# Optimization experiments

Measured on AMD Instinct MI355X. Metric: run time of the kernel, lower is better.

Reference implementation:

```python
import jax, jax.numpy as jnp
import numpy as np

N = 100000   # total nodes (batched graphs)
E = 800000   # random edges (self-loops appended -> E+N total)
G = 2000     # number of graphs in batch
H = 4        # heads per GAT layer
D = 64       # hidden_size (per-head out dim)
IN = 64      # in_feats
EXTRA = 8    # extra graph-level feats
HID = H * D  # 256


def setup_inputs() -> dict:
    key = jax.random.key(0)
    ks = jax.random.split(key, 24)
    s = 0.5  # init std used in the torch module
    feats_node = jax.random.normal(ks[0], (N, IN), jnp.float32)
    feats_graph = jax.random.normal(ks[1], (G, EXTRA), jnp.float32)
    # edges + self loops (DGL GATConv requires no zero-in-degree nodes)
    src = jnp.concatenate([jax.random.randint(ks[2], (E,), 0, N), jnp.arange(N)])
    dst = jnp.concatenate([jax.random.randint(ks[3], (E,), 0, N), jnp.arange(N)])
    node_gid = jnp.sort(jax.random.randint(ks[4], (N,), 0, G))
    # GAT layer 1
    W1 = jax.random.normal(ks[5], (IN, HID), jnp.float32) * s
    al1 = jax.random.normal(ks[6], (H, D), jnp.float32) * s
    ar1 = jax.random.normal(ks[7], (H, D), jnp.float32) * s
    b1 = jnp.zeros((HID,), jnp.float32)
    # GAT layer 2
    W2 = jax.random.normal(ks[8], (HID, HID), jnp.float32) * s
    al2 = jax.random.normal(ks[9], (H, D), jnp.float32) * s
    ar2 = jax.random.normal(ks[10], (H, D), jnp.float32) * s
    b2 = jnp.zeros((HID,), jnp.float32)
    # WeightedAverage readout score
    Ws = jax.random.normal(ks[11], (HID, 1), jnp.float32) * s
    bs = jnp.zeros((1,), jnp.float32)
    # MLP: 264 -> 128 -> 64 -> 1 with SELU
    Wm1 = jax.random.normal(ks[12], (HID + EXTRA, 2 * D), jnp.float32) * s
    bm1 = jnp.zeros((2 * D,), jnp.float32)
    Wm2 = jax.random.normal(ks[13], (2 * D, D), jnp.float32) * s
    bm2 = jnp.zeros((D,), jnp.float32)
    Wm3 = jax.random.normal(ks[14], (D, 1), jnp.float32) * s
    bm3 = jnp.zeros((1,), jnp.float32)
    return dict(feats_node=feats_node, feats_graph=feats_graph,
                W1=W1, al1=al1, ar1=ar1, b1=b1,
                W2=W2, al2=al2, ar2=ar2, b2=b2,
                Ws=Ws, bs=bs, Wm1=Wm1, bm1=bm1, Wm2=Wm2, bm2=bm2,
                Wm3=Wm3, bm3=bm3,
                src=src, dst=dst, node_gid=node_gid)


def gat_layer(x, W, al, ar, b, src, dst):
    # DGL GATConv: fc -> per-node attn projections -> edge leaky_relu ->
    # edge softmax over incoming edges -> weighted scatter-sum -> +bias
    f = (x @ W).reshape(N, H, D)                       # [N,H,D]
    el = jnp.einsum('nhd,hd->nh', f, al)               # [N,H]
    er = jnp.einsum('nhd,hd->nh', f, ar)               # [N,H]
    e = jax.nn.leaky_relu(el[src] + er[dst], 0.2)      # [E',H]
    m = jax.ops.segment_max(e, dst, num_segments=N)    # per-dst max
    e = jnp.exp(e - m[dst])
    denom = jax.ops.segment_sum(e, dst, num_segments=N)
    alpha = e / denom[dst]                             # edge softmax [E',H]
    out = jax.ops.segment_sum(alpha[:, :, None] * f[src], dst, num_segments=N)
    return out.reshape(N, HID) + b


def reference(feats_node, feats_graph, W1, al1, ar1, b1, W2, al2, ar2, b2,
              Ws, bs, Wm1, bm1, Wm2, bm2, Wm3, bm3, src, dst, node_gid):
    x = jax.nn.relu(gat_layer(feats_node, W1, al1, ar1, b1, src, dst))
    x = jax.nn.relu(gat_layer(x, W2, al2, ar2, b2, src, dst))
    # weighted-average readout per graph: sum(w*x)/sum(w)
    w = jax.nn.sigmoid(x @ Ws + bs)                    # [N,1]
    num = jax.ops.segment_sum(w * x, node_gid, num_segments=G)
    den = jax.ops.segment_sum(w, node_gid, num_segments=G)
    emb = num / jnp.where(den == 0, 1.0, den)          # [G,HID]
    h = jnp.concatenate([emb, feats_graph], axis=1)    # [G,HID+EXTRA]
    h = jax.nn.selu(h @ Wm1 + bm1)
    h = jax.nn.selu(h @ Wm2 + bm2)
    return h @ Wm3 + bm3                               # [G,1]
```

## Files before the change

kernel.cpp:

```cpp
#include <hip/hip_runtime.h>
#include <hip/hip_bf16.h>
#include <math.h>

#define NN     100000
#define GG     2000
#define HH     4
#define DD     64
#define HID    256
#define INF_   64
#define EXTRA  8

typedef unsigned short u16;
typedef __attribute__((ext_vector_type(8))) short bf16x8;
typedef __attribute__((ext_vector_type(4))) float f32x4;

__device__ __forceinline__ u16 f2bf(float f) {
    unsigned u = __float_as_uint(f);
    return (u16)((u + 0x7fffu + ((u >> 16) & 1u)) >> 16);
}
__device__ __forceinline__ float bf2f(u16 v) {
    return __uint_as_float(((unsigned)v) << 16);
}

__global__ __launch_bounds__(256) void wsplit_kernel(
    const float* __restrict__ W, u16* __restrict__ hi, u16* __restrict__ lo,
    int K, int lgK)
{
    int idx = blockIdx.x * 256 + threadIdx.x;
    if (idx >= 256 * K) return;
    int n = idx >> lgK, k = idx & (K - 1);
    float w = W[k * HID + n];
    u16 h = f2bf(w);
    hi[idx] = h;
    lo[idx] = f2bf(w - bf2f(h));
}

template<bool BF16_OUT>
__global__ __launch_bounds__(256) void mfma_gemm_kernel(
    const float* __restrict__ A, const u16* __restrict__ BThi,
    const u16* __restrict__ BTlo, float* __restrict__ Cf, u16* __restrict__ Cb,
    const float* __restrict__ al, const float* __restrict__ ar,
    float* __restrict__ el, float* __restrict__ er, int M, int K)
{
    __shared__ __align__(16) u16 Ah[128 * 40];
    __shared__ __align__(16) u16 Al[128 * 40];
    __shared__ __align__(16) u16 Bh[128 * 40];
    __shared__ __align__(16) u16 Bl[128 * 40];
    const int tid  = threadIdx.x;
    const int wave = tid >> 6, lane = tid & 63;
    const int quad = lane >> 4, l15 = lane & 15;
    const int wy = wave >> 1, wx = wave & 1;
    const int r0 = blockIdx.x * 128, c0 = blockIdx.y * 128;
    const int sr = tid >> 2, sseg = tid & 3;

    f32x4 acc[4][4];
    #pragma unroll
    for (int i = 0; i < 4; ++i)
        #pragma unroll
        for (int j = 0; j < 4; ++j)
            acc[i][j] = (f32x4){0.f, 0.f, 0.f, 0.f};

    for (int k0 = 0; k0 < K; k0 += 32) {
        #pragma unroll
        for (int half = 0; half < 2; ++half) {
            int r = sr + half * 64;
            int gr = min(r0 + r, M - 1);
            const float* ap = A + (size_t)gr * K + k0 + sseg * 8;
            float4 va0 = *reinterpret_cast<const float4*>(ap);
            float4 va1 = *reinterpret_cast<const float4*>(ap + 4);
            float av[8] = {va0.x, va0.y, va0.z, va0.w, va1.x, va1.y, va1.z, va1.w};
            bf16x8 vh, vl;
            #pragma unroll
            for (int m = 0; m < 8; ++m) {
                u16 h = f2bf(av[m]);
                vh[m] = (short)h;
                vl[m] = (short)f2bf(av[m] - bf2f(h));
            }
            *reinterpret_cast<bf16x8*>(&Ah[r * 40 + sseg * 8]) = vh;
            *reinterpret_cast<bf16x8*>(&Al[r * 40 + sseg * 8]) = vl;
            int gc = c0 + r;
            *reinterpret_cast<bf16x8*>(&Bh[r * 40 + sseg * 8]) =
                *reinterpret_cast<const bf16x8*>(BThi + (size_t)gc * K + k0 + sseg * 8);
            *reinterpret_cast<bf16x8*>(&Bl[r * 40 + sseg * 8]) =
                *reinterpret_cast<const bf16x8*>(BTlo + (size_t)gc * K + k0 + sseg * 8);
        }
        __syncthreads();
        bf16x8 afh[4], afl[4], bfh[4], bfl[4];
        #pragma unroll
        for (int i = 0; i < 4; ++i) {
            int row = (wy * 64 + i * 16 + l15) * 40 + quad * 8;
            afh[i] = *reinterpret_cast<const bf16x8*>(&Ah[row]);
            afl[i] = *reinterpret_cast<const bf16x8*>(&Al[row]);
        }
        #pragma unroll
        for (int j = 0; j < 4; ++j) {
            int row = (wx * 64 + j * 16 + l15) * 40 + quad * 8;
            bfh[j] = *reinterpret_cast<const bf16x8*>(&Bh[row]);
            bfl[j] = *reinterpret_cast<const bf16x8*>(&Bl[row]);
        }
        #pragma unroll
        for (int i = 0; i < 4; ++i)
            #pragma unroll
            for (int j = 0; j < 4; ++j) {
                acc[i][j] = __builtin_amdgcn_mfma_f32_16x16x32_bf16(afh[i], bfh[j], acc[i][j], 0, 0, 0);
                acc[i][j] = __builtin_amdgcn_mfma_f32_16x16x32_bf16(afl[i], bfh[j], acc[i][j], 0, 0, 0);
                acc[i][j] = __builtin_amdgcn_mfma_f32_16x16x32_bf16(afh[i], bfl[j], acc[i][j], 0, 0, 0);
            }
        __syncthreads();
    }

    #pragma unroll
    for (int i = 0; i < 4; ++i)
        #pragma unroll
        for (int rr = 0; rr < 4; ++rr) {
            int grow = r0 + wy * 64 + i * 16 + quad * 4 + rr;
            if (grow < M) {
                if (BF16_OUT) {
                    u16* crow = Cb + (size_t)grow * HID + c0 + wx * 64 + l15;
                    #pragma unroll
                    for (int j = 0; j < 4; ++j) crow[j * 16] = f2bf(acc[i][j][rr]);
                } else {
                    float* crow = Cf + (size_t)grow * HID + c0 + wx * 64 + l15;
                    #pragma unroll
                    for (int j = 0; j < 4; ++j) crow[j * 16] = acc[i][j][rr];
                }
            }
        }

    const int h = blockIdx.y * 2 + wx;
    float alf[4], arf[4];
    #pragma unroll
    for (int j = 0; j < 4; ++j) {
        alf[j] = al[h * DD + j * 16 + l15];
        arf[j] = ar[h * DD + j * 16 + l15];
    }
    #pragma unroll
    for (int i = 0; i < 4; ++i)
        #pragma unroll
        for (int rr = 0; rr < 4; ++rr) {
            float sl = acc[i][0][rr] * alf[0] + acc[i][1][rr] * alf[1]
                     + acc[i][2][rr] * alf[2] + acc[i][3][rr] * alf[3];
            float sr_ = acc[i][0][rr] * arf[0] + acc[i][1][rr] * arf[1]
                      + acc[i][2][rr] * arf[2] + acc[i][3][rr] * arf[3];
            #pragma unroll
            for (int off = 1; off < 16; off <<= 1) {
                sl  += __shfl_xor(sl, off, 64);
                sr_ += __shfl_xor(sr_, off, 64);
            }
            if (l15 == 0) {
                int grow = r0 + wy * 64 + i * 16 + quad * 4 + rr;
                if (grow < M) {
                    el[grow * 4 + h] = sl;
                    er[grow * 4 + h] = sr_;
                }
            }
        }
}

__device__ __forceinline__ float leaky02(float x) { return x > 0.f ? x : 0.2f * x; }

__global__ __launch_bounds__(256) void edge_softmax_kernel(
    const float* __restrict__ el, const float* __restrict__ er,
    const int* __restrict__ rowptr, const int* __restrict__ colsrc,
    float* __restrict__ w, float* __restrict__ invden)
{
    int idx = blockIdx.x * 256 + threadIdx.x;
    if (idx >= NN * HH) return;
    int t = idx >> 2, h = idx & 3;
    int beg = rowptr[t], end = rowptr[t + 1];
    float ert = er[idx];
    float m = -1e30f;
    for (int i = beg; i < end; ++i) {
        int s = colsrc[i];
        m = fmaxf(m, leaky02(el[s * 4 + h] + ert));
    }
    float den = 0.f;
    for (int i = beg; i < end; ++i) {
        int s = colsrc[i];
        float v = expf(leaky02(el[s * 4 + h] + ert) - m);
        w[(size_t)i * 4 + h] = v;
        den += v;
    }
    invden[idx] = 1.f / den;
}

__global__ __launch_bounds__(256) void aggregate_f32_kernel(
    const float* __restrict__ F, const float* __restrict__ w,
    const float* __restrict__ invden, const int* __restrict__ rowptr,
    const int* __restrict__ colsrc, const float* __restrict__ bias,
    float* __restrict__ out)
{
    int t = blockIdx.x * 4 + (threadIdx.x >> 6);
    int lane = threadIdx.x & 63;
    if (t >= NN) return;
    int beg = rowptr[t], end = rowptr[t + 1];
    const int h = lane >> 4;
    float4 acc0 = make_float4(0.f, 0.f, 0.f, 0.f);
    float4 acc1 = make_float4(0.f, 0.f, 0.f, 0.f);
    int i = beg;
    for (; i + 1 < end; i += 2) {
        int s0 = colsrc[i], s1 = colsrc[i + 1];
        float w0 = w[(size_t)i * 4 + h];
        float w1 = w[(size_t)(i + 1) * 4 + h];
        float4 f0 = *reinterpret_cast<const float4*>(F + (size_t)s0 * HID + 4 * lane);
        float4 f1 = *reinterpret_cast<const float4*>(F + (size_t)s1 * HID + 4 * lane);
        acc0.x += w0 * f0.x; acc0.y += w0 * f0.y; acc0.z += w0 * f0.z; acc0.w += w0 * f0.w;
        acc1.x += w1 * f1.x; acc1.y += w1 * f1.y; acc1.z += w1 * f1.z; acc1.w += w1 * f1.w;
    }
    if (i < end) {
        int s0 = colsrc[i];
        float w0 = w[(size_t)i * 4 + h];
        float4 f0 = *reinterpret_cast<const float4*>(F + (size_t)s0 * HID + 4 * lane);
        acc0.x += w0 * f0.x; acc0.y += w0 * f0.y; acc0.z += w0 * f0.z; acc0.w += w0 * f0.w;
    }
    float inv = invden[t * 4 + h];
    float4 bv = *reinterpret_cast<const float4*>(bias + 4 * lane);
    float4 r;
    r.x = fmaxf((acc0.x + acc1.x) * inv + bv.x, 0.f);
    r.y = fmaxf((acc0.y + acc1.y) * inv + bv.y, 0.f);
    r.z = fmaxf((acc0.z + acc1.z) * inv + bv.z, 0.f);
    r.w = fmaxf((acc0.w + acc1.w) * inv + bv.w, 0.f);
    *reinterpret_cast<float4*>(out + (size_t)t * HID + 4 * lane) = r;
}

__global__ __launch_bounds__(256) void aggregate_bf16_kernel(
    const u16* __restrict__ F, const float* __restrict__ w,
    const float* __restrict__ invden, const int* __restrict__ rowptr,
    const int* __restrict__ colsrc, const float* __restrict__ bias,
    u16* __restrict__ out)
{
    int t = blockIdx.x * 4 + (threadIdx.x >> 6);
    int lane = threadIdx.x & 63;
    if (t >= NN) return;
    int beg = rowptr[t], end = rowptr[t + 1];
    const int h = lane >> 4;
    float4 acc0 = make_float4(0.f, 0.f, 0.f, 0.f);
    float4 acc1 = make_float4(0.f, 0.f, 0.f, 0.f);
    int i = beg;
    for (; i + 1 < end; i += 2) {
        int s0 = colsrc[i], s1 = colsrc[i + 1];
        float w0 = w[(size_t)i * 4 + h];
        float w1 = w[(size_t)(i + 1) * 4 + h];
        ushort4 f0 = *reinterpret_cast<const ushort4*>(F + (size_t)s0 * HID + 4 * lane);
        ushort4 f1 = *reinterpret_cast<const ushort4*>(F + (size_t)s1 * HID + 4 * lane);
        acc0.x += w0 * bf2f(f0.x); acc0.y += w0 * bf2f(f0.y);
        acc0.z += w0 * bf2f(f0.z); acc0.w += w0 * bf2f(f0.w);
        acc1.x += w1 * bf2f(f1.x); acc1.y += w1 * bf2f(f1.y);
        acc1.z += w1 * bf2f(f1.z); acc1.w += w1 * bf2f(f1.w);
    }
    if (i < end) {
        int s0 = colsrc[i];
        float w0 = w[(size_t)i * 4 + h];
        ushort4 f0 = *reinterpret_cast<const ushort4*>(F + (size_t)s0 * HID + 4 * lane);
        acc0.x += w0 * bf2f(f0.x); acc0.y += w0 * bf2f(f0.y);
        acc0.z += w0 * bf2f(f0.z); acc0.w += w0 * bf2f(f0.w);
    }
    float inv = invden[t * 4 + h];
    float4 bv = *reinterpret_cast<const float4*>(bias + 4 * lane);
    ushort4 r;
    r.x = f2bf(fmaxf((acc0.x + acc1.x) * inv + bv.x, 0.f));
    r.y = f2bf(fmaxf((acc0.y + acc1.y) * inv + bv.y, 0.f));
    r.z = f2bf(fmaxf((acc0.z + acc1.z) * inv + bv.z, 0.f));
    r.w = f2bf(fmaxf((acc0.w + acc1.w) * inv + bv.w, 0.f));
    *reinterpret_cast<ushort4*>(out + (size_t)t * HID + 4 * lane) = r;
}

__global__ __launch_bounds__(256) void readout_kernel(
    const u16* __restrict__ X, const float* __restrict__ Ws,
    const float* __restrict__ bs, const int* __restrict__ gptr,
    float* __restrict__ emb)
{
    int g = blockIdx.x * 4 + (threadIdx.x >> 6);
    int lane = threadIdx.x & 63;
    if (g >= GG) return;
    int beg = gptr[g], end = gptr[g + 1];
    float4 wv = *reinterpret_cast<const float4*>(Ws + 4 * lane);
    float b = bs[0];
    float4 acc = make_float4(0.f, 0.f, 0.f, 0.f);
    float wsum = 0.f;
    for (int n = beg; n < end; ++n) {
        ushort4 xv = *reinterpret_cast<const ushort4*>(X + (size_t)n * HID + 4 * lane);
        float x0 = bf2f(xv.x), x1 = bf2f(xv.y), x2 = bf2f(xv.z), x3 = bf2f(xv.w);
        float p = x0 * wv.x + x1 * wv.y + x2 * wv.z + x3 * wv.w;
        #pragma unroll
        for (int off = 32; off; off >>= 1) p += __shfl_xor(p, off, 64);
        float w = 1.f / (1.f + expf(-(p + b)));
        wsum += w;
        acc.x += w * x0; acc.y += w * x1; acc.z += w * x2; acc.w += w * x3;
    }
    float inv = (wsum == 0.f) ? 1.f : wsum;
    float4 e;
    e.x = acc.x / inv; e.y = acc.y / inv; e.z = acc.z / inv; e.w = acc.w / inv;
    *reinterpret_cast<float4*>(emb + (size_t)g * HID + 4 * lane) = e;
}

__device__ __forceinline__ float selu_f(float x)
{
    const float scale = 1.0507009873554805f, alpha = 1.6732632423543772f;
    return scale * (x > 0.f ? x : alpha * expm1f(x));
}

__global__ __launch_bounds__(128) void mlp_kernel(
    const float* __restrict__ emb, const float* __restrict__ fg,
    const float* __restrict__ Wm1, const float* __restrict__ bm1,
    const float* __restrict__ Wm2, const float* __restrict__ bm2,
    const float* __restrict__ Wm3, const float* __restrict__ bm3,
    float* __restrict__ out)
{
    int g = blockIdx.x;
    __shared__ float h[HID + EXTRA];
    __shared__ float h1[128];
    __shared__ float h2[64];
    int tid = threadIdx.x;
    h[tid] = emb[(size_t)g * HID + tid];
    h[128 + tid] = emb[(size_t)g * HID + 128 + tid];
    if (tid < EXTRA) h[HID + tid] = fg[(size_t)g * EXTRA + tid];
    __syncthreads();
    float acc = bm1[tid];
    for (int i = 0; i < HID + EXTRA; ++i) acc += h[i] * Wm1[i * 128 + tid];
    h1[tid] = selu_f(acc);
    __syncthreads();
    if (tid < 64) {
        float acc2 = bm2[tid];
        for (int i = 0; i < 128; ++i) acc2 += h1[i] * Wm2[i * 64 + tid];
        h2[tid] = selu_f(acc2);
    }
    __syncthreads();
    if (tid < 64) {
        float p = h2[tid] * Wm3[tid];
        #pragma unroll
        for (int off = 32; off; off >>= 1) p += __shfl_xor(p, off, 64);
        if (tid == 0) out[g] = p + bm3[0];
    }
}

__global__ void count_dst_kernel(const int* __restrict__ dst, int* __restrict__ cnt, int E)
{
    int e = blockIdx.x * 256 + threadIdx.x;
    if (e < E) atomicAdd(&cnt[dst[e]], 1);
}
__global__ void count_gid_kernel(const int* __restrict__ gid, int* __restrict__ cnt, int n)
{
    int i = blockIdx.x * 256 + threadIdx.x;
    if (i < n) atomicAdd(&cnt[gid[i]], 1);
}
__global__ void fill_csr_kernel(const int* __restrict__ src, const int* __restrict__ dst,
                                int* __restrict__ cursor, int* __restrict__ colsrc, int E)
{
    int e = blockIdx.x * 256 + threadIdx.x;
    if (e < E) {
        int p = atomicAdd(&cursor[dst[e]], 1);
        colsrc[p] = src[e];
    }
}

__global__ __launch_bounds__(256) void scan_blocks_kernel(
    const int* __restrict__ in, int n, int* __restrict__ out, int* __restrict__ partials)
{
    __shared__ int lds[256];
    int tid = threadIdx.x;
    int base = blockIdx.x * 1024 + tid * 4;
    int v0 = (base + 0 < n) ? in[base + 0] : 0;
    int v1 = (base + 1 < n) ? in[base + 1] : 0;
    int v2 = (base + 2 < n) ? in[base + 2] : 0;
    int v3 = (base + 3 < n) ? in[base + 3] : 0;
    int s = v0 + v1 + v2 + v3;
    lds[tid] = s;
    __syncthreads();
    for (int off = 1; off < 256; off <<= 1) {
        int t = (tid >= off) ? lds[tid - off] : 0;
        __syncthreads();
        lds[tid] += t;
        __syncthreads();
    }
    int excl = lds[tid] - s;
    if (base + 0 < n) out[base + 0] = excl;
    if (base + 1 < n) out[base + 1] = excl + v0;
    if (base + 2 < n) out[base + 2] = excl + v0 + v1;
    if (base + 3 < n) out[base + 3] = excl + v0 + v1 + v2;
    if (tid == 255) partials[blockIdx.x] = lds[255];
}

__global__ __launch_bounds__(256) void scan_partials_kernel(int* partials, int nb)
{
    __shared__ int lds[256];
    int tid = threadIdx.x;
    int v = (tid < nb) ? partials[tid] : 0;
    lds[tid] = v;
    __syncthreads();
    for (int off = 1; off < 256; off <<= 1) {
        int t = (tid >= off) ? lds[tid - off] : 0;
        __syncthreads();
        lds[tid] += t;
        __syncthreads();
    }
    int excl = lds[tid] - v;
    if (tid < nb) partials[tid] = excl;
}

__global__ void add_offsets_kernel(int* __restrict__ out, const int* __restrict__ partials, int n)
{
    int i = blockIdx.x * 256 + threadIdx.x;
    if (i < n) out[i] += partials[i >> 10];
}

extern "C" void kernel_launch(void* const* d_in, const int* in_sizes, int n_in,
                              void* d_out, int out_size, void* d_ws, size_t ws_size,
                              hipStream_t stream)
{
    const float* feats_node  = (const float*)d_in[0];
    const float* feats_graph = (const float*)d_in[1];
    const float* W1  = (const float*)d_in[2];
    const float* al1 = (const float*)d_in[3];
    const float* ar1 = (const float*)d_in[4];
    const float* b1  = (const float*)d_in[5];
    const float* W2  = (const float*)d_in[6];
    const float* al2 = (const float*)d_in[7];
    const float* ar2 = (const float*)d_in[8];
    const float* b2  = (const float*)d_in[9];
    const float* Ws  = (const float*)d_in[10];
    const float* bs  = (const float*)d_in[11];
    const float* Wm1 = (const float*)d_in[12];
    const float* bm1 = (const float*)d_in[13];
    const float* Wm2 = (const float*)d_in[14];
    const float* bm2 = (const float*)d_in[15];
    const float* Wm3 = (const float*)d_in[16];
    const float* bm3 = (const float*)d_in[17];
    const int* src = (const int*)d_in[18];
    const int* dst = (const int*)d_in[19];
    const int* gid = (const int*)d_in[20];
    float* out = (float*)d_out;
    const int E = in_sizes[18];

    char* p = (char*)d_ws;
    auto alloc = [&](size_t bytes) {
        char* r = p;
        p += (bytes + 255) & ~(size_t)255;
        return r;
    };
    float* F      = (float*)alloc((size_t)NN * HID * 4);
    float* X      = (float*)alloc((size_t)NN * HID * 4);
    float* el     = (float*)alloc((size_t)NN * HH * 4);
    float* er     = (float*)alloc((size_t)NN * HH * 4);
    float* wbuf   = (float*)alloc((size_t)E * HH * 4);
    float* invden = (float*)alloc((size_t)NN * HH * 4);
    int*   cnt    = (int*)alloc((size_t)(NN + 1) * 4);
    int*   rowptr = (int*)alloc((size_t)(NN + 1) * 4);
    int*   colsrc = (int*)alloc((size_t)E * 4);
    int*   gcnt   = (int*)alloc((size_t)(GG + 1) * 4);
    int*   gptr   = (int*)alloc((size_t)(GG + 1) * 4);
    int*   parts  = (int*)alloc(1024 * 4);
    float* emb    = (float*)alloc((size_t)GG * HID * 4);
    u16*   BT1h   = (u16*)alloc((size_t)HID * INF_ * 2);
    u16*   BT1l   = (u16*)alloc((size_t)HID * INF_ * 2);
    u16*   BT2h   = (u16*)alloc((size_t)HID * HID * 2);
    u16*   BT2l   = (u16*)alloc((size_t)HID * HID * 2);
    u16*   Fbf2   = (u16*)F;
    u16*   Xbf2   = (u16*)X;

    hipMemsetAsync(cnt, 0, (size_t)(NN + 1) * 4, stream);
    count_dst_kernel<<<(E + 255) / 256, 256, 0, stream>>>(dst, cnt, E);
    {
        int n = NN + 1, nb = (n + 1023) / 1024;
        scan_blocks_kernel<<<nb, 256, 0, stream>>>(cnt, n, rowptr, parts);
        scan_partials_kernel<<<1, 256, 0, stream>>>(parts, nb);
        add_offsets_kernel<<<(n + 255) / 256, 256, 0, stream>>>(rowptr, parts, n);
    }
    hipMemcpyAsync(cnt, rowptr, (size_t)(NN + 1) * 4, hipMemcpyDeviceToDevice, stream);
    fill_csr_kernel<<<(E + 255) / 256, 256, 0, stream>>>(src, dst, cnt, colsrc, E);

    hipMemsetAsync(gcnt, 0, (size_t)(GG + 1) * 4, stream);
    count_gid_kernel<<<(NN + 255) / 256, 256, 0, stream>>>(gid, gcnt, NN);
    {
        int n = GG + 1, nb = (n + 1023) / 1024;
        scan_blocks_kernel<<<nb, 256, 0, stream>>>(gcnt, n, gptr, parts);
        scan_partials_kernel<<<1, 256, 0, stream>>>(parts, nb);
        add_offsets_kernel<<<(n + 255) / 256, 256, 0, stream>>>(gptr, parts, n);
    }

    wsplit_kernel<<<(HID * INF_ + 255) / 256, 256, 0, stream>>>(W1, BT1h, BT1l, INF_, 6);
    wsplit_kernel<<<(HID * HID + 255) / 256, 256, 0, stream>>>(W2, BT2h, BT2l, HID, 8);

    dim3 ggrid((NN + 127) / 128, HID / 128);
    const int nh_blocks = (NN * HH + 255) / 256;

    mfma_gemm_kernel<false><<<ggrid, 256, 0, stream>>>(
        feats_node, BT1h, BT1l, F, nullptr, al1, ar1, el, er, NN, INF_);
    edge_softmax_kernel<<<nh_blocks, 256, 0, stream>>>(el, er, rowptr, colsrc, wbuf, invden);
    aggregate_f32_kernel<<<(NN + 3) / 4, 256, 0, stream>>>(F, wbuf, invden, rowptr, colsrc, b1, X);

    mfma_gemm_kernel<true><<<ggrid, 256, 0, stream>>>(
        X, BT2h, BT2l, nullptr, Fbf2, al2, ar2, el, er, NN, HID);
    edge_softmax_kernel<<<nh_blocks, 256, 0, stream>>>(el, er, rowptr, colsrc, wbuf, invden);
    aggregate_bf16_kernel<<<(NN + 3) / 4, 256, 0, stream>>>(Fbf2, wbuf, invden, rowptr, colsrc,
                                                            b2, Xbf2);

    readout_kernel<<<(GG + 3) / 4, 256, 0, stream>>>(Xbf2, Ws, bs, gptr, emb);
    mlp_kernel<<<GG, 128, 0, stream>>>(emb, feats_graph, Wm1, bm1, Wm2, bm2, Wm3, bm3, out);
}
```

Baseline: 671.6 us.

## Aggregate raw 64-wide features before layer-1 projection and fold attention into weights

Layer 1 is reordered so attention logits are computed directly from input features using W1·al and W1·ar precomputed vectors. Neighbor aggregation then gathers 64-float input rows instead of 256-float projected rows, producing per-head aggregated inputs. A new per-head MFMA GEMM applies W1 with bias and ReLU afterwards. This cuts gather traffic in the first aggregation about fourfold, at the cost of writing and re-reading a full 256-wide intermediate and adding a few kernels.

```diff
diff --git a/kernel.cpp b/kernel.cpp
--- a/kernel.cpp
+++ b/kernel.cpp
@@ -33,6 +33,143 @@
     u16 h = f2bf(w);
     hi[idx] = h;
     lo[idx] = f2bf(w - bf2f(h));
+}
+
+__global__ __launch_bounds__(256) void walprep_kernel(
+    const float* __restrict__ W1, const float* __restrict__ al,
+    const float* __restrict__ ar, float* __restrict__ wal, float* __restrict__ war)
+{
+    int tid = threadIdx.x;
+    int d = tid >> 2, h = tid & 3;
+    const float* wrow = W1 + d * HID + h * DD;
+    const float* av = al + h * DD;
+    const float* bv = ar + h * DD;
+    float s1 = 0.f, s2 = 0.f;
+    for (int c = 0; c < DD; ++c) { s1 += wrow[c] * av[c]; s2 += wrow[c] * bv[c]; }
+    wal[d * 4 + h] = s1;
+    war[d * 4 + h] = s2;
+}
+
+__global__ __launch_bounds__(256) void elr1_kernel(
+    const float* __restrict__ feats, const float* __restrict__ wal,
+    const float* __restrict__ war, float* __restrict__ el, float* __restrict__ er)
+{
+    int idx = blockIdx.x * 256 + threadIdx.x;
+    if (idx >= NN * HH) return;
+    int n = idx >> 2, h = idx & 3;
+    const float* f = feats + (size_t)n * INF_;
+    float s1 = 0.f, s2 = 0.f;
+    #pragma unroll 4
+    for (int d = 0; d < INF_; d += 4) {
+        float4 fv = *reinterpret_cast<const float4*>(f + d);
+        s1 += fv.x * wal[(d + 0) * 4 + h] + fv.y * wal[(d + 1) * 4 + h]
+            + fv.z * wal[(d + 2) * 4 + h] + fv.w * wal[(d + 3) * 4 + h];
+        s2 += fv.x * war[(d + 0) * 4 + h] + fv.y * war[(d + 1) * 4 + h]
+            + fv.z * war[(d + 2) * 4 + h] + fv.w * war[(d + 3) * 4 + h];
+    }
+    el[idx] = s1;
+    er[idx] = s2;
+}
+
+__global__ __launch_bounds__(256) void aggregate_feats_kernel(
+    const float* __restrict__ feats, const float* __restrict__ w,
+    const float* __restrict__ invden, const int* __restrict__ rowptr,
+    const int* __restrict__ colsrc, float* __restrict__ Y1)
+{
+    int t = blockIdx.x * 4 + (threadIdx.x >> 6);
+    int lane = threadIdx.x & 63;
+    if (t >= NN) return;
+    int beg = rowptr[t], end = rowptr[t + 1];
+    float a0 = 0.f, a1 = 0.f, a2 = 0.f, a3 = 0.f;
+    float b0 = 0.f, b1 = 0.f, b2 = 0.f, b3 = 0.f;
+    int i = beg;
+    for (; i + 1 < end; i += 2) {
+        int s0 = colsrc[i], s1 = colsrc[i + 1];
+        float4 w0 = *reinterpret_cast<const float4*>(w + (size_t)i * 4);
+        float4 w1 = *reinterpret_cast<const float4*>(w + (size_t)(i + 1) * 4);
+        float f0 = feats[(size_t)s0 * INF_ + lane];
+        float f1 = feats[(size_t)s1 * INF_ + lane];
+        a0 += w0.x * f0; a1 += w0.y * f0; a2 += w0.z * f0; a3 += w0.w * f0;
+        b0 += w1.x * f1; b1 += w1.y * f1; b2 += w1.z * f1; b3 += w1.w * f1;
+    }
+    if (i < end) {
+        int s0 = colsrc[i];
+        float4 w0 = *reinterpret_cast<const float4*>(w + (size_t)i * 4);
+        float f0 = feats[(size_t)s0 * INF_ + lane];
+        a0 += w0.x * f0; a1 += w0.y * f0; a2 += w0.z * f0; a3 += w0.w * f0;
+    }
+    float4 inv = *reinterpret_cast<const float4*>(invden + (size_t)t * 4);
+    float* y = Y1 + (size_t)t * HID;
+    y[lane]       = (a0 + b0) * inv.x;
+    y[64 + lane]  = (a1 + b1) * inv.y;
+    y[128 + lane] = (a2 + b2) * inv.z;
+    y[192 + lane] = (a3 + b3) * inv.w;
+}
+
+__global__ __launch_bounds__(256) void gemm_head_kernel(
+    const float* __restrict__ Y1, const u16* __restrict__ BThi,
+    const u16* __restrict__ BTlo, const float* __restrict__ bias,
+    float* __restrict__ X1, int M)
+{
+    const int tid  = threadIdx.x;
+    const int wv   = tid >> 6, lane = tid & 63;
+    const int quad = lane >> 4, l15 = lane & 15;
+    const int r0 = blockIdx.x * 128;
+    const int cbase = wv * 64;
+
+    f32x4 acc[8][4];
+    #pragma unroll
+    for (int i = 0; i < 8; ++i)
+        #pragma unroll
+        for (int j = 0; j < 4; ++j)
+            acc[i][j] = (f32x4){0.f, 0.f, 0.f, 0.f};
+
+    #pragma unroll
+    for (int k0 = 0; k0 < 64; k0 += 32) {
+        bf16x8 bh[4], bl[4];
+        #pragma unroll
+        for (int j = 0; j < 4; ++j) {
+            int n = cbase + j * 16 + l15;
+            bh[j] = *reinterpret_cast<const bf16x8*>(BThi + (size_t)n * 64 + k0 + quad * 8);
+            bl[j] = *reinterpret_cast<const bf16x8*>(BTlo + (size_t)n * 64 + k0 + quad * 8);
+        }
+        #pragma unroll
+        for (int i = 0; i < 8; ++i) {
+            int gr = min(r0 + i * 16 + l15, M - 1);
+            const float* ap = Y1 + (size_t)gr * HID + cbase + k0 + quad * 8;
+            float4 va0 = *reinterpret_cast<const float4*>(ap);
+            float4 va1 = *reinterpret_cast<const float4*>(ap + 4);
+            float av[8] = {va0.x, va0.y, va0.z, va0.w, va1.x, va1.y, va1.z, va1.w};
+            bf16x8 vh, vl;
+            #pragma unroll
+            for (int m = 0; m < 8; ++m) {
+                u16 h = f2bf(av[m]);
+                vh[m] = (short)h;
+                vl[m] = (short)f2bf(av[m] - bf2f(h));
+            }
+            #pragma unroll
+            for (int j = 0; j < 4; ++j) {
+                acc[i][j] = __builtin_amdgcn_mfma_f32_16x16x32_bf16(vh, bh[j], acc[i][j], 0, 0, 0);
+                acc[i][j] = __builtin_amdgcn_mfma_f32_16x16x32_bf16(vl, bh[j], acc[i][j], 0, 0, 0);
+                acc[i][j] = __builtin_amdgcn_mfma_f32_16x16x32_bf16(vh, bl[j], acc[i][j], 0, 0, 0);
+            }
+        }
+    }
+    float bv[4];
+    #pragma unroll
+    for (int j = 0; j < 4; ++j) bv[j] = bias[cbase + j * 16 + l15];
+    #pragma unroll
+    for (int i = 0; i < 8; ++i)
+        #pragma unroll
+        for (int rr = 0; rr < 4; ++rr) {
+            int grow = r0 + i * 16 + quad * 4 + rr;
+            if (grow < M) {
+                float* xrow = X1 + (size_t)grow * HID + cbase + l15;
+                #pragma unroll
+                for (int j = 0; j < 4; ++j)
+                    xrow[j * 16] = fmaxf(acc[i][j][rr] + bv[j], 0.f);
+            }
+        }
 }
 
 template<bool BF16_OUT>
@@ -182,45 +319,6 @@
         den += v;
     }
     invden[idx] = 1.f / den;
-}
-
-__global__ __launch_bounds__(256) void aggregate_f32_kernel(
-    const float* __restrict__ F, const float* __restrict__ w,
-    const float* __restrict__ invden, const int* __restrict__ rowptr,
-    const int* __restrict__ colsrc, const float* __restrict__ bias,
-    float* __restrict__ out)
-{
-    int t = blockIdx.x * 4 + (threadIdx.x >> 6);
-    int lane = threadIdx.x & 63;
-    if (t >= NN) return;
-    int beg = rowptr[t], end = rowptr[t + 1];
-    const int h = lane >> 4;
-    float4 acc0 = make_float4(0.f, 0.f, 0.f, 0.f);
-    float4 acc1 = make_float4(0.f, 0.f, 0.f, 0.f);
-    int i = beg;
-    for (; i + 1 < end; i += 2) {
-        int s0 = colsrc[i], s1 = colsrc[i + 1];
-        float w0 = w[(size_t)i * 4 + h];
-        float w1 = w[(size_t)(i + 1) * 4 + h];
-        float4 f0 = *reinterpret_cast<const float4*>(F + (size_t)s0 * HID + 4 * lane);
-        float4 f1 = *reinterpret_cast<const float4*>(F + (size_t)s1 * HID + 4 * lane);
-        acc0.x += w0 * f0.x; acc0.y += w0 * f0.y; acc0.z += w0 * f0.z; acc0.w += w0 * f0.w;
-        acc1.x += w1 * f1.x; acc1.y += w1 * f1.y; acc1.z += w1 * f1.z; acc1.w += w1 * f1.w;
-    }
-    if (i < end) {
-        int s0 = colsrc[i];
-        float w0 = w[(size_t)i * 4 + h];
-        float4 f0 = *reinterpret_cast<const float4*>(F + (size_t)s0 * HID + 4 * lane);
-        acc0.x += w0 * f0.x; acc0.y += w0 * f0.y; acc0.z += w0 * f0.z; acc0.w += w0 * f0.w;
-    }
-    float inv = invden[t * 4 + h];
-    float4 bv = *reinterpret_cast<const float4*>(bias + 4 * lane);
-    float4 r;
-    r.x = fmaxf((acc0.x + acc1.x) * inv + bv.x, 0.f);
-    r.y = fmaxf((acc0.y + acc1.y) * inv + bv.y, 0.f);
-    r.z = fmaxf((acc0.z + acc1.z) * inv + bv.z, 0.f);
-    r.w = fmaxf((acc0.w + acc1.w) * inv + bv.w, 0.f);
-    *reinterpret_cast<float4*>(out + (size_t)t * HID + 4 * lane) = r;
 }
 
 __global__ __launch_bounds__(256) void aggregate_bf16_kernel(
@@ -438,7 +536,7 @@
         p += (bytes + 255) & ~(size_t)255;
         return r;
     };
-    float* F      = (float*)alloc((size_t)NN * HID * 4);
+    float* Y1     = (float*)alloc((size_t)NN * HID * 4);
     float* X      = (float*)alloc((size_t)NN * HID * 4);
     float* el     = (float*)alloc((size_t)NN * HH * 4);
     float* er     = (float*)alloc((size_t)NN * HH * 4);
@@ -455,7 +553,9 @@
     u16*   BT1l   = (u16*)alloc((size_t)HID * INF_ * 2);
     u16*   BT2h   = (u16*)alloc((size_t)HID * HID * 2);
     u16*   BT2l   = (u16*)alloc((size_t)HID * HID * 2);
-    u16*   Fbf2   = (u16*)F;
+    float* wal1   = (float*)alloc(INF_ * HH * 4);
+    float* war1   = (float*)alloc(INF_ * HH * 4);
+    u16*   Fbf2   = (u16*)Y1;
     u16*   Xbf2   = (u16*)X;
 
     hipMemsetAsync(cnt, 0, (size_t)(NN + 1) * 4, stream);
@@ -480,15 +580,17 @@
 
     wsplit_kernel<<<(HID * INF_ + 255) / 256, 256, 0, stream>>>(W1, BT1h, BT1l, INF_, 6);
     wsplit_kernel<<<(HID * HID + 255) / 256, 256, 0, stream>>>(W2, BT2h, BT2l, HID, 8);
+    walprep_kernel<<<1, 256, 0, stream>>>(W1, al1, ar1, wal1, war1);
+
+    const int nh_blocks = (NN * HH + 255) / 256;
+
+    elr1_kernel<<<nh_blocks, 256, 0, stream>>>(feats_node, wal1, war1, el, er);
+    edge_softmax_kernel<<<nh_blocks, 256, 0, stream>>>(el, er, rowptr, colsrc, wbuf, invden);
+    aggregate_feats_kernel<<<(NN + 3) / 4, 256, 0, stream>>>(feats_node, wbuf, invden,
+                                                             rowptr, colsrc, Y1);
+    gemm_head_kernel<<<(NN + 127) / 128, 256, 0, stream>>>(Y1, BT1h, BT1l, b1, X, NN);
 
     dim3 ggrid((NN + 127) / 128, HID / 128);
-    const int nh_blocks = (NN * HH + 255) / 256;
-
-    mfma_gemm_kernel<false><<<ggrid, 256, 0, stream>>>(
-        feats_node, BT1h, BT1l, F, nullptr, al1, ar1, el, er, NN, INF_);
-    edge_softmax_kernel<<<nh_blocks, 256, 0, stream>>>(el, er, rowptr, colsrc, wbuf, invden);
-    aggregate_f32_kernel<<<(NN + 3) / 4, 256, 0, stream>>>(F, wbuf, invden, rowptr, colsrc, b1, X);
-
     mfma_gemm_kernel<true><<<ggrid, 256, 0, stream>>>(
         X, BT2h, BT2l, nullptr, Fbf2, al2, ar2, el, er, NN, HID);
     edge_softmax_kernel<<<nh_blocks, 256, 0, stream>>>(el, er, rowptr, colsrc, wbuf, invden);
```

After: 645.4 us. 3.9% less time.
